# Kernel tuning notes

Measured on AMD Instinct MI355X. Metric: run time of the kernel, lower is better.

## Reference

```python
import jax, jax.numpy as jnp
import numpy as np

DIM = 768
HEADS = 12
HEAD_DIM = DIM // HEADS
SCALE = HEAD_DIM ** -0.5


def setup_inputs() -> dict:
    key = jax.random.key(0)
    k1, k2, k3, k4 = jax.random.split(key, 4)
    x = jax.random.normal(k1, (1, 4096, DIM), dtype=jnp.float32)
    # qkv: Linear(dim, 3*dim), bias=False
    W_qkv = jax.random.normal(k2, (DIM, 3 * DIM), dtype=jnp.float32) * (DIM ** -0.5)
    # proj: Linear(dim, dim) with bias
    W_proj = jax.random.normal(k3, (DIM, DIM), dtype=jnp.float32) * (DIM ** -0.5)
    b_proj = jax.random.normal(k4, (DIM,), dtype=jnp.float32) * 0.01
    return {"x": x, "W_qkv": W_qkv, "W_proj": W_proj, "b_proj": b_proj}


def reference(x, W_qkv, W_proj, b_proj):
    b, n, d = x.shape
    qkv = x @ W_qkv                                  # [b, n, 3d]
    q, k, v = jnp.split(qkv, 3, axis=-1)             # each [b, n, d]
    # split heads: [b, n, (h hd)] -> [b, h, n, hd]
    def heads(t):
        return t.reshape(b, n, HEADS, HEAD_DIM).transpose(0, 2, 1, 3)
    q, k, v = heads(q) * SCALE, heads(k), heads(v)
    sim = jnp.einsum('bhid,bhjd->bhij', q, k)        # [b, h, n, n] -- full score matrix
    attn = jax.nn.softmax(sim, axis=-1)
    out = jnp.einsum('bhij,bhjd->bhid', attn, v)     # [b, h, n, hd]
    out = out.transpose(0, 2, 1, 3).reshape(b, n, d)  # merge heads
    return out @ W_proj + b_proj
```

## Files before the change

kernel.cpp:

```cpp
#include <hip/hip_runtime.h>
#include <math.h>

#define TOKENS 4096
#define DMODEL 768
#define NHEADS 12
#define HDIM   64
#define QKV_N  2304
#define ATTN_SCALE 0.125f
#define QSCALE_LOG2E (0.125f * 1.44269504088896340736f)

typedef __attribute__((ext_vector_type(8))) short bf16x8;
typedef __attribute__((ext_vector_type(4))) float floatx4;

__device__ __forceinline__ ushort f2bf(float f) {
    union { float f; unsigned u; } cv; cv.f = f;
    unsigned u = cv.u;
    u += 0x7fffu + ((u >> 16) & 1u);
    return (ushort)(u >> 16);
}

__device__ __forceinline__ unsigned pack_bf16_rne(float a, float b) {
    union { float f; unsigned u; } ca, cb; ca.f = a; cb.f = b;
    unsigned ua = ca.u + 0x7fffu + ((ca.u >> 16) & 1u);
    unsigned ub = cb.u + 0x7fffu + ((cb.u >> 16) & 1u);
    return __builtin_amdgcn_perm(ub, ua, 0x07060302);
}

__device__ __forceinline__ void gl2lds16(const ushort* g, ushort* l) {
    __builtin_amdgcn_global_load_lds(
        (const __attribute__((address_space(1))) void*)g,
        (__attribute__((address_space(3))) void*)l, 16, 0, 0);
}

__device__ __forceinline__ bf16x8 frag(const ushort* ls, int row, int chunk) {
    return *(const bf16x8*)(ls + row * 64 + ((chunk ^ (row & 7)) * 8));
}

__global__ __launch_bounds__(256) void cvt_bf16_kernel(
    const float* __restrict__ in, ushort* __restrict__ out, int n4)
{
    const int i = blockIdx.x * 256 + threadIdx.x;
    if (i < n4) {
        const float4 v = ((const float4*)in)[i];
        ushort4 h;
        h.x = f2bf(v.x); h.y = f2bf(v.y); h.z = f2bf(v.z); h.w = f2bf(v.w);
        ((ushort4*)out)[i] = h;
    }
}

__global__ __launch_bounds__(256) void transpose_cvt_kernel(
    const float* __restrict__ in, ushort* __restrict__ out, int R, int C)
{
    __shared__ ushort tile[32][33];
    const int tx  = threadIdx.x & 31;
    const int ty8 = threadIdx.x >> 5;
    const int c0 = blockIdx.x * 32;
    const int r0 = blockIdx.y * 32;
    #pragma unroll
    for (int p = 0; p < 4; ++p) {
        const int r = ty8 + p * 8;
        tile[r][tx] = f2bf(in[(size_t)(r0 + r) * C + c0 + tx]);
    }
    __syncthreads();
    #pragma unroll
    for (int p = 0; p < 4; ++p) {
        const int c = ty8 + p * 8;
        out[(size_t)(c0 + c) * R + r0 + tx] = tile[tx][c];
    }
}

template<int NT>
__device__ __forceinline__ void gemm_body_async(
    const ushort* __restrict__ A, const ushort* __restrict__ Bt, int K,
    int m0, int n0, floatx4 acc[4][NT], ushort* ls)
{
    ushort* lsA = ls;
    ushort* lsB = ls + 8192;

    const int tid  = threadIdx.x;
    const int lane = tid & 63;
    const int wave = tid >> 6;
    const int wm = wave >> 1, wn = wave & 1;
    const int quad = lane >> 4, l16 = lane & 15;

    const int lrow = lane >> 3;
    const int csw  = ((lane & 7) ^ lrow) * 8;

    const ushort* gA = A  + (size_t)(m0 + wave * 32 + lrow) * K + csw;
    const ushort* gB = Bt + (size_t)(n0 + wave * NT * 8 + lrow) * K + csw;
    ushort* lA = lsA + (wave * 32) * 64;
    ushort* lB = lsB + (wave * NT * 8) * 64;

    for (int k0 = 0; k0 < K; k0 += 64) {
        __syncthreads();
        #pragma unroll
        for (int p = 0; p < 4; ++p)
            gl2lds16(gA + (size_t)p * 8 * K + k0, lA + p * 8 * 64);
        #pragma unroll
        for (int p = 0; p < NT; ++p)
            gl2lds16(gB + (size_t)p * 8 * K + k0, lB + p * 8 * 64);
        __syncthreads();

        #pragma unroll
        for (int ks = 0; ks < 2; ++ks) {
            bf16x8 af[4], bfr[NT];
            #pragma unroll
            for (int mt = 0; mt < 4; ++mt)
                af[mt] = frag(lsA, wm * 64 + mt * 16 + l16, ks * 4 + quad);
            #pragma unroll
            for (int nt = 0; nt < NT; ++nt)
                bfr[nt] = frag(lsB, wn * NT * 16 + nt * 16 + l16, ks * 4 + quad);
            #pragma unroll
            for (int mt = 0; mt < 4; ++mt)
                #pragma unroll
                for (int nt = 0; nt < NT; ++nt)
                    acc[mt][nt] = __builtin_amdgcn_mfma_f32_16x16x32_bf16(
                        af[mt], bfr[nt], acc[mt][nt], 0, 0, 0);
        }
    }
}

__global__ __launch_bounds__(256) void gemm_qkv_mfma(
    const ushort* __restrict__ Xb, const ushort* __restrict__ Wt,
    ushort* __restrict__ Qb, ushort* __restrict__ Kb, ushort* __restrict__ Vt)
{
    __shared__ __align__(16) ushort ls[16384];
    const int m0 = blockIdx.y * 128;
    const int n0 = blockIdx.x * 128;

    floatx4 acc[4][4] = {};
    gemm_body_async<4>(Xb, Wt, DMODEL, m0, n0, acc, ls);

    const int tid  = threadIdx.x;
    const int lane = tid & 63;
    const int wave = tid >> 6;
    const int wm = wave >> 1, wn = wave & 1;
    const int quad = lane >> 4, l16 = lane & 15;

    if (n0 < 2 * DMODEL) {
        const float scale = (n0 < DMODEL) ? QSCALE_LOG2E : 1.0f;
        ushort* outp = (n0 < DMODEL) ? Qb : Kb;
        const int colg = (n0 < DMODEL) ? n0 : n0 - DMODEL;
        #pragma unroll
        for (int p = 0; p < 2; ++p) {
            __syncthreads();
            if (wm == p) {
                #pragma unroll
                for (int mt = 0; mt < 4; ++mt)
                    #pragma unroll
                    for (int nt = 0; nt < 4; ++nt) {
                        const int row = mt * 16 + quad * 4;
                        const int col = wn * 64 + nt * 16 + l16;
                        #pragma unroll
                        for (int r = 0; r < 4; ++r)
                            ls[(row + r) * 136 + col] = f2bf(acc[mt][nt][r] * scale);
                    }
            }
            __syncthreads();
            #pragma unroll
            for (int p2 = 0; p2 < 4; ++p2) {
                const int row = (tid >> 4) + p2 * 16;
                const int c8  = (tid & 15) * 8;
                *(uint4*)(outp + (size_t)(m0 + p * 64 + row) * DMODEL + colg + c8) =
                    *(const uint4*)(ls + row * 136 + c8);
            }
        }
    } else {
        const int hd0 = n0 - 2 * DMODEL;
        #pragma unroll
        for (int p = 0; p < 2; ++p) {
            __syncthreads();
            if (wn == p) {
                #pragma unroll
                for (int mt = 0; mt < 4; ++mt)
                    #pragma unroll
                    for (int nt = 0; nt < 4; ++nt) {
                        const int hd  = nt * 16 + l16;
                        const int tok = wm * 64 + mt * 16 + quad * 4;
                        #pragma unroll
                        for (int r = 0; r < 4; ++r)
                            ls[hd * 136 + tok + r] = f2bf(acc[mt][nt][r]);
                    }
            }
            __syncthreads();
            #pragma unroll
            for (int p2 = 0; p2 < 4; ++p2) {
                const int row = (tid >> 4) + p2 * 16;
                const int c8  = (tid & 15) * 8;
                *(uint4*)(Vt + (size_t)(hd0 + p * 64 + row) * TOKENS + m0 + c8) =
                    *(const uint4*)(ls + row * 136 + c8);
            }
        }
    }
}

__global__ __launch_bounds__(256) void gemm_proj_mfma(
    const ushort* __restrict__ Ab, const ushort* __restrict__ Wt,
    const float* __restrict__ bias, float* __restrict__ out)
{
    __shared__ __align__(16) ushort ls[12288];
    const int m0 = blockIdx.y * 128;
    const int n0 = blockIdx.x * 64;

    floatx4 acc[4][2] = {};
    gemm_body_async<2>(Ab, Wt, DMODEL, m0, n0, acc, ls);

    const int lane = threadIdx.x & 63;
    const int wave = threadIdx.x >> 6;
    const int wm = wave >> 1, wn = wave & 1;
    const int quad = lane >> 4, l16 = lane & 15;
    const int row0 = m0 + wm * 64 + quad * 4;
    const int col0 = n0 + wn * 32;

    #pragma unroll
    for (int nt = 0; nt < 2; ++nt) {
        const int col = col0 + nt * 16 + l16;
        const float bv = bias[col];
        #pragma unroll
        for (int mt = 0; mt < 4; ++mt)
            #pragma unroll
            for (int r = 0; r < 4; ++r)
                out[(size_t)(row0 + mt * 16 + r) * DMODEL + col] =
                    acc[mt][nt][r] + bv;
    }
}

__global__ __launch_bounds__(256) void attn_mfma_kernel(
    const ushort* __restrict__ Qb, const ushort* __restrict__ Kb,
    const ushort* __restrict__ Vt, ushort* __restrict__ attn_out)
{
    __shared__ __align__(16) ushort lds[20480];

    const int tid  = threadIdx.x;
    const int wave = tid >> 6;
    const int lane = tid & 63;
    const int quad = lane >> 4;
    const int l16  = lane & 15;
    const int sw   = (l16 & 7);
    const int h    = blockIdx.y;
    const int i0   = blockIdx.x * 64;

    const ushort* qbase = Qb + (size_t)(i0 + wave * 16 + l16) * DMODEL + h * HDIM;
    const bf16x8 qf0 = *(const bf16x8*)(qbase + quad * 8);
    const bf16x8 qf1 = *(const bf16x8*)(qbase + 32 + quad * 8);

    bf16x8 ones;
    #pragma unroll
    for (int i = 0; i < 8; ++i) ones[i] = (short)0x3F80;

    floatx4 O[4] = {{0.f,0.f,0.f,0.f},{0.f,0.f,0.f,0.f},{0.f,0.f,0.f,0.f},{0.f,0.f,0.f,0.f}};
    floatx4 Ol = {0.f, 0.f, 0.f, 0.f};

    ushort* pw = lds + 16384 + wave * 1024 + l16 * 64;

    const int lrow = lane >> 3;
    const int csw  = ((lane & 7) ^ lrow) * 8;
    const ushort* gK = Kb + (size_t)(wave * 16 + lrow) * DMODEL + h * HDIM + csw;
    const ushort* gV = Vt + (size_t)(h * HDIM + wave * 16 + lrow) * TOKENS + csw;

    #pragma unroll
    for (int p = 0; p < 2; ++p) {
        gl2lds16(gK + (size_t)p * 8 * DMODEL, lds + (wave * 16 + p * 8) * 64);
        gl2lds16(gV + (size_t)p * 8 * TOKENS, lds + 8192 + (wave * 16 + p * 8) * 64);
    }

    for (int j0 = 0; j0 < TOKENS; j0 += 64) {
        const int cur = (j0 >> 6) & 1;
        ushort* Ks = lds + cur * 4096;
        ushort* Vs = lds + 8192 + cur * 4096;
        ushort* Kn = lds + (1 - cur) * 4096;
        ushort* Vn = lds + 8192 + (1 - cur) * 4096;

        __syncthreads();

        if (j0 + 64 < TOKENS) {
            #pragma unroll
            for (int p = 0; p < 2; ++p) {
                gl2lds16(gK + (size_t)(j0 + 64) * DMODEL + (size_t)p * 8 * DMODEL,
                         Kn + (wave * 16 + p * 8) * 64);
                gl2lds16(gV + (size_t)(j0 + 64) + (size_t)p * 8 * TOKENS,
                         Vn + (wave * 16 + p * 8) * 64);
            }
        }

        floatx4 Sv[4];
        #pragma unroll
        for (int jt = 0; jt < 4; ++jt) {
            const bf16x8 k0 = frag(Ks, jt * 16 + l16, quad);
            const bf16x8 k1 = frag(Ks, jt * 16 + l16, 4 + quad);
            floatx4 s = {0.f, 0.f, 0.f, 0.f};
            s = __builtin_amdgcn_mfma_f32_16x16x32_bf16(k0, qf0, s, 0, 0, 0);
            s = __builtin_amdgcn_mfma_f32_16x16x32_bf16(k1, qf1, s, 0, 0, 0);
            Sv[jt] = s;
        }

        #pragma unroll
        for (int jt = 0; jt < 4; ++jt) {
            const float p0 = __builtin_amdgcn_exp2f(Sv[jt][0]);
            const float p1 = __builtin_amdgcn_exp2f(Sv[jt][1]);
            const float p2 = __builtin_amdgcn_exp2f(Sv[jt][2]);
            const float p3 = __builtin_amdgcn_exp2f(Sv[jt][3]);
            uint2 val;
            val.x = pack_bf16_rne(p0, p1);
            val.y = pack_bf16_rne(p2, p3);
            const int chunk = jt * 2 + (quad >> 1);
            *(uint2*)(pw + ((chunk ^ sw) * 8) + (quad & 1) * 4) = val;
        }

        const bf16x8 pf0 = *(const bf16x8*)(pw + ((quad ^ sw) * 8));
        const bf16x8 pf1 = *(const bf16x8*)(pw + (((4 + quad) ^ sw) * 8));

        Ol = __builtin_amdgcn_mfma_f32_16x16x32_bf16(pf0, ones, Ol, 0, 0, 0);
        Ol = __builtin_amdgcn_mfma_f32_16x16x32_bf16(pf1, ones, Ol, 0, 0, 0);

        #pragma unroll
        for (int nt = 0; nt < 4; ++nt) {
            const bf16x8 v0 = frag(Vs, nt * 16 + l16, quad);
            const bf16x8 v1 = frag(Vs, nt * 16 + l16, 4 + quad);
            O[nt] = __builtin_amdgcn_mfma_f32_16x16x32_bf16(pf0, v0, O[nt], 0, 0, 0);
            O[nt] = __builtin_amdgcn_mfma_f32_16x16x32_bf16(pf1, v1, O[nt], 0, 0, 0);
        }
    }

    float linv[4];
    #pragma unroll
    for (int r = 0; r < 4; ++r) linv[r] = __builtin_amdgcn_rcpf(Ol[r]);

    const int orow0 = i0 + wave * 16 + quad * 4;
    #pragma unroll
    for (int nt = 0; nt < 4; ++nt) {
        const int d = h * HDIM + nt * 16 + l16;
        #pragma unroll
        for (int r = 0; r < 4; ++r)
            attn_out[(size_t)(orow0 + r) * DMODEL + d] = f2bf(O[nt][r] * linv[r]);
    }
}

extern "C" void kernel_launch(void* const* d_in, const int* in_sizes, int n_in,
                              void* d_out, int out_size, void* d_ws, size_t ws_size,
                              hipStream_t stream)
{
    const float* x     = (const float*)d_in[0];
    const float* Wqkv  = (const float*)d_in[1];
    const float* Wproj = (const float*)d_in[2];
    const float* bproj = (const float*)d_in[3];
    float* out = (float*)d_out;

    ushort* Xb     = (ushort*)d_ws;
    ushort* WqkvT  = Xb    + (size_t)TOKENS * DMODEL;
    ushort* WprojT = WqkvT + (size_t)QKV_N * DMODEL;
    ushort* Qb     = WprojT + (size_t)DMODEL * DMODEL;
    ushort* Kb     = Qb    + (size_t)TOKENS * DMODEL;
    ushort* Vt     = Kb    + (size_t)TOKENS * DMODEL;
    ushort* attn   = Vt    + (size_t)TOKENS * DMODEL;

    cvt_bf16_kernel<<<dim3(TOKENS * DMODEL / 4 / 256), 256, 0, stream>>>(
        x, Xb, TOKENS * DMODEL / 4);
    transpose_cvt_kernel<<<dim3(QKV_N / 32, DMODEL / 32), 256, 0, stream>>>(
        Wqkv, WqkvT, DMODEL, QKV_N);
    transpose_cvt_kernel<<<dim3(DMODEL / 32, DMODEL / 32), 256, 0, stream>>>(
        Wproj, WprojT, DMODEL, DMODEL);

    gemm_qkv_mfma<<<dim3(QKV_N / 128, TOKENS / 128), 256, 0, stream>>>(
        Xb, WqkvT, Qb, Kb, Vt);

    attn_mfma_kernel<<<dim3(TOKENS / 64, NHEADS), 256, 0, stream>>>(
        Qb, Kb, Vt, attn);

    gemm_proj_mfma<<<dim3(DMODEL / 64, TOKENS / 128), 256, 0, stream>>>(
        attn, WprojT, bproj, out);
}
```

Before: 214.9 us.

## Restructure attention so one wave processes all 64 query rows per block

The attention kernel now launches single-wave blocks. Each wave handles all four 16-row query tiles, so every K and V fragment read from LDS is reused across four query tiles instead of one. Block-level __syncthreads is replaced by explicit s_waitcnt vmcnt waits on the asynchronous global-to-LDS copies, since only one wave touches the shared buffers. The cost is fewer resident waves (768 in total), more registers per wave and less latency hiding, which may leave SIMDs underused.

```diff
diff --git a/kernel.cpp b/kernel.cpp
--- a/kernel.cpp
+++ b/kernel.cpp
@@ -225,114 +225,140 @@
     }
 }
 
-__global__ __launch_bounds__(256) void attn_mfma_kernel(
+__global__ __launch_bounds__(64) void attn_mfma_kernel(
     const ushort* __restrict__ Qb, const ushort* __restrict__ Kb,
     const ushort* __restrict__ Vt, ushort* __restrict__ attn_out)
 {
     __shared__ __align__(16) ushort lds[20480];
 
-    const int tid  = threadIdx.x;
-    const int wave = tid >> 6;
-    const int lane = tid & 63;
+    const int lane = threadIdx.x;
     const int quad = lane >> 4;
     const int l16  = lane & 15;
-    const int sw   = (l16 & 7);
     const int h    = blockIdx.y;
     const int i0   = blockIdx.x * 64;
 
-    const ushort* qbase = Qb + (size_t)(i0 + wave * 16 + l16) * DMODEL + h * HDIM;
-    const bf16x8 qf0 = *(const bf16x8*)(qbase + quad * 8);
-    const bf16x8 qf1 = *(const bf16x8*)(qbase + 32 + quad * 8);
+    bf16x8 qf[4][2];
+    #pragma unroll
+    for (int qt = 0; qt < 4; ++qt)
+        #pragma unroll
+        for (int ks = 0; ks < 2; ++ks)
+            qf[qt][ks] = *(const bf16x8*)(Qb +
+                (size_t)(i0 + qt * 16 + l16) * DMODEL + h * HDIM + ks * 32 + quad * 8);
 
     bf16x8 ones;
     #pragma unroll
     for (int i = 0; i < 8; ++i) ones[i] = (short)0x3F80;
 
-    floatx4 O[4] = {{0.f,0.f,0.f,0.f},{0.f,0.f,0.f,0.f},{0.f,0.f,0.f,0.f},{0.f,0.f,0.f,0.f}};
-    floatx4 Ol = {0.f, 0.f, 0.f, 0.f};
-
-    ushort* pw = lds + 16384 + wave * 1024 + l16 * 64;
+    floatx4 O[4][4];
+    #pragma unroll
+    for (int mt = 0; mt < 4; ++mt)
+        #pragma unroll
+        for (int nt = 0; nt < 4; ++nt) O[mt][nt] = (floatx4){0.f, 0.f, 0.f, 0.f};
+    floatx4 Ol[4];
+    #pragma unroll
+    for (int mt = 0; mt < 4; ++mt) Ol[mt] = (floatx4){0.f, 0.f, 0.f, 0.f};
+
+    ushort* Pb = lds + 16384;
 
     const int lrow = lane >> 3;
     const int csw  = ((lane & 7) ^ lrow) * 8;
-    const ushort* gK = Kb + (size_t)(wave * 16 + lrow) * DMODEL + h * HDIM + csw;
-    const ushort* gV = Vt + (size_t)(h * HDIM + wave * 16 + lrow) * TOKENS + csw;
-
-    #pragma unroll
-    for (int p = 0; p < 2; ++p) {
-        gl2lds16(gK + (size_t)p * 8 * DMODEL, lds + (wave * 16 + p * 8) * 64);
-        gl2lds16(gV + (size_t)p * 8 * TOKENS, lds + 8192 + (wave * 16 + p * 8) * 64);
+    const ushort* gK = Kb + (size_t)lrow * DMODEL + h * HDIM + csw;
+    const ushort* gV = Vt + (size_t)(h * HDIM + lrow) * TOKENS + csw;
+
+    #pragma unroll
+    for (int p = 0; p < 8; ++p) {
+        gl2lds16(gK + (size_t)p * 8 * DMODEL, lds + p * 8 * 64);
+        gl2lds16(gV + (size_t)p * 8 * TOKENS, lds + 8192 + p * 8 * 64);
     }
 
     for (int j0 = 0; j0 < TOKENS; j0 += 64) {
         const int cur = (j0 >> 6) & 1;
-        ushort* Ks = lds + cur * 4096;
-        ushort* Vs = lds + 8192 + cur * 4096;
-        ushort* Kn = lds + (1 - cur) * 4096;
-        ushort* Vn = lds + 8192 + (1 - cur) * 4096;
-
-        __syncthreads();
+        const ushort* Ks = lds + cur * 4096;
+        const ushort* Vs = lds + 8192 + cur * 4096;
 
         if (j0 + 64 < TOKENS) {
-            #pragma unroll
-            for (int p = 0; p < 2; ++p) {
+            ushort* Kn = lds + (1 - cur) * 4096;
+            ushort* Vn = lds + 8192 + (1 - cur) * 4096;
+            #pragma unroll
+            for (int p = 0; p < 8; ++p) {
                 gl2lds16(gK + (size_t)(j0 + 64) * DMODEL + (size_t)p * 8 * DMODEL,
-                         Kn + (wave * 16 + p * 8) * 64);
+                         Kn + p * 8 * 64);
                 gl2lds16(gV + (size_t)(j0 + 64) + (size_t)p * 8 * TOKENS,
-                         Vn + (wave * 16 + p * 8) * 64);
-            }
-        }
-
-        floatx4 Sv[4];
+                         Vn + p * 8 * 64);
+            }
+            asm volatile("s_waitcnt vmcnt(16)" ::: "memory");
+        } else {
+            asm volatile("s_waitcnt vmcnt(0)" ::: "memory");
+        }
+
+        floatx4 Sv[4][4];
         #pragma unroll
         for (int jt = 0; jt < 4; ++jt) {
             const bf16x8 k0 = frag(Ks, jt * 16 + l16, quad);
             const bf16x8 k1 = frag(Ks, jt * 16 + l16, 4 + quad);
-            floatx4 s = {0.f, 0.f, 0.f, 0.f};
-            s = __builtin_amdgcn_mfma_f32_16x16x32_bf16(k0, qf0, s, 0, 0, 0);
-            s = __builtin_amdgcn_mfma_f32_16x16x32_bf16(k1, qf1, s, 0, 0, 0);
-            Sv[jt] = s;
-        }
-
-        #pragma unroll
-        for (int jt = 0; jt < 4; ++jt) {
-            const float p0 = __builtin_amdgcn_exp2f(Sv[jt][0]);
-            const float p1 = __builtin_amdgcn_exp2f(Sv[jt][1]);
-            const float p2 = __builtin_amdgcn_exp2f(Sv[jt][2]);
-            const float p3 = __builtin_amdgcn_exp2f(Sv[jt][3]);
-            uint2 val;
-            val.x = pack_bf16_rne(p0, p1);
-            val.y = pack_bf16_rne(p2, p3);
-            const int chunk = jt * 2 + (quad >> 1);
-            *(uint2*)(pw + ((chunk ^ sw) * 8) + (quad & 1) * 4) = val;
-        }
-
-        const bf16x8 pf0 = *(const bf16x8*)(pw + ((quad ^ sw) * 8));
-        const bf16x8 pf1 = *(const bf16x8*)(pw + (((4 + quad) ^ sw) * 8));
-
-        Ol = __builtin_amdgcn_mfma_f32_16x16x32_bf16(pf0, ones, Ol, 0, 0, 0);
-        Ol = __builtin_amdgcn_mfma_f32_16x16x32_bf16(pf1, ones, Ol, 0, 0, 0);
+            #pragma unroll
+            for (int qt = 0; qt < 4; ++qt) {
+                floatx4 s = {0.f, 0.f, 0.f, 0.f};
+                s = __builtin_amdgcn_mfma_f32_16x16x32_bf16(k0, qf[qt][0], s, 0, 0, 0);
+                s = __builtin_amdgcn_mfma_f32_16x16x32_bf16(k1, qf[qt][1], s, 0, 0, 0);
+                Sv[jt][qt] = s;
+            }
+        }
+
+        #pragma unroll
+        for (int jt = 0; jt < 4; ++jt)
+            #pragma unroll
+            for (int qt = 0; qt < 4; ++qt) {
+                const float p0 = __builtin_amdgcn_exp2f(Sv[jt][qt][0]);
+                const float p1 = __builtin_amdgcn_exp2f(Sv[jt][qt][1]);
+                const float p2 = __builtin_amdgcn_exp2f(Sv[jt][qt][2]);
+                const float p3 = __builtin_amdgcn_exp2f(Sv[jt][qt][3]);
+                uint2 val;
+                val.x = pack_bf16_rne(p0, p1);
+                val.y = pack_bf16_rne(p2, p3);
+                const int q = qt * 16 + l16;
+                const int c = jt * 2 + (quad >> 1);
+                *(uint2*)(Pb + (q * 8 + (c ^ (q & 7))) * 8 + (quad & 1) * 4) = val;
+            }
+
+        bf16x8 pf[4][2];
+        #pragma unroll
+        for (int mt = 0; mt < 4; ++mt) {
+            pf[mt][0] = frag(Pb, mt * 16 + l16, quad);
+            pf[mt][1] = frag(Pb, mt * 16 + l16, 4 + quad);
+        }
+
+        #pragma unroll
+        for (int mt = 0; mt < 4; ++mt) {
+            Ol[mt] = __builtin_amdgcn_mfma_f32_16x16x32_bf16(pf[mt][0], ones, Ol[mt], 0, 0, 0);
+            Ol[mt] = __builtin_amdgcn_mfma_f32_16x16x32_bf16(pf[mt][1], ones, Ol[mt], 0, 0, 0);
+        }
 
         #pragma unroll
         for (int nt = 0; nt < 4; ++nt) {
             const bf16x8 v0 = frag(Vs, nt * 16 + l16, quad);
             const bf16x8 v1 = frag(Vs, nt * 16 + l16, 4 + quad);
-            O[nt] = __builtin_amdgcn_mfma_f32_16x16x32_bf16(pf0, v0, O[nt], 0, 0, 0);
-            O[nt] = __builtin_amdgcn_mfma_f32_16x16x32_bf16(pf1, v1, O[nt], 0, 0, 0);
-        }
-    }
-
-    float linv[4];
-    #pragma unroll
-    for (int r = 0; r < 4; ++r) linv[r] = __builtin_amdgcn_rcpf(Ol[r]);
-
-    const int orow0 = i0 + wave * 16 + quad * 4;
-    #pragma unroll
-    for (int nt = 0; nt < 4; ++nt) {
-        const int d = h * HDIM + nt * 16 + l16;
-        #pragma unroll
-        for (int r = 0; r < 4; ++r)
-            attn_out[(size_t)(orow0 + r) * DMODEL + d] = f2bf(O[nt][r] * linv[r]);
+            #pragma unroll
+            for (int mt = 0; mt < 4; ++mt) {
+                O[mt][nt] = __builtin_amdgcn_mfma_f32_16x16x32_bf16(pf[mt][0], v0, O[mt][nt], 0, 0, 0);
+                O[mt][nt] = __builtin_amdgcn_mfma_f32_16x16x32_bf16(pf[mt][1], v1, O[mt][nt], 0, 0, 0);
+            }
+        }
+    }
+
+    #pragma unroll
+    for (int mt = 0; mt < 4; ++mt) {
+        float linv[4];
+        #pragma unroll
+        for (int r = 0; r < 4; ++r) linv[r] = __builtin_amdgcn_rcpf(Ol[mt][r]);
+        const int row0 = i0 + mt * 16 + quad * 4;
+        #pragma unroll
+        for (int nt = 0; nt < 4; ++nt) {
+            const int d = h * HDIM + nt * 16 + l16;
+            #pragma unroll
+            for (int r = 0; r < 4; ++r)
+                attn_out[(size_t)(row0 + r) * DMODEL + d] = f2bf(O[mt][nt][r] * linv[r]);
+        }
     }
 }
 
@@ -364,7 +390,7 @@
     gemm_qkv_mfma<<<dim3(QKV_N / 128, TOKENS / 128), 256, 0, stream>>>(
         Xb, WqkvT, Qb, Kb, Vt);
 
-    attn_mfma_kernel<<<dim3(TOKENS / 64, NHEADS), 256, 0, stream>>>(
+    attn_mfma_kernel<<<dim3(TOKENS / 64, NHEADS), 64, 0, stream>>>(
         Qb, Kb, Vt, attn);
 
     gemm_proj_mfma<<<dim3(DMODEL / 64, TOKENS / 128), 256, 0, stream>>>(
```

Measured after the change: 240.4 us. 11.9% more time.

## Keep P in registers using 16x16x16 MFMA and permuted V layout in LDS

Applied to the files above, without the earlier changes.

The attention kernel no longer round-trips the softmax probabilities through LDS. The exp'd scores stay in registers as bf16x4 fragments and feed 16x16x16 bf16 MFMAs directly. To match that operand layout, V tiles are loaded through registers and scattered into a permuted, padded LDS layout (row stride 68) instead of using direct global-to-LDS copies. This removes the P write/read and one LDS buffer, but it doubles the MFMA count at half the K depth and adds register-staged V stores plus a sync placed at the end of each iteration.

```diff
diff --git a/kernel.cpp b/kernel.cpp
--- a/kernel.cpp
+++ b/kernel.cpp
@@ -10,6 +10,7 @@
 #define QSCALE_LOG2E (0.125f * 1.44269504088896340736f)
 
 typedef __attribute__((ext_vector_type(8))) short bf16x8;
+typedef __attribute__((ext_vector_type(4))) short bf16x4;
 typedef __attribute__((ext_vector_type(4))) float floatx4;
 
 __device__ __forceinline__ ushort f2bf(float f) {
@@ -229,14 +230,13 @@
     const ushort* __restrict__ Qb, const ushort* __restrict__ Kb,
     const ushort* __restrict__ Vt, ushort* __restrict__ attn_out)
 {
-    __shared__ __align__(16) ushort lds[20480];
+    __shared__ __align__(16) ushort lds[16896];
 
     const int tid  = threadIdx.x;
     const int wave = tid >> 6;
     const int lane = tid & 63;
     const int quad = lane >> 4;
     const int l16  = lane & 15;
-    const int sw   = (l16 & 7);
     const int h    = blockIdx.y;
     const int i0   = blockIdx.x * 64;
 
@@ -244,43 +244,55 @@
     const bf16x8 qf0 = *(const bf16x8*)(qbase + quad * 8);
     const bf16x8 qf1 = *(const bf16x8*)(qbase + 32 + quad * 8);
 
-    bf16x8 ones;
-    #pragma unroll
-    for (int i = 0; i < 8; ++i) ones[i] = (short)0x3F80;
+    bf16x4 ones4;
+    #pragma unroll
+    for (int i = 0; i < 4; ++i) ones4[i] = (short)0x3F80;
 
     floatx4 O[4] = {{0.f,0.f,0.f,0.f},{0.f,0.f,0.f,0.f},{0.f,0.f,0.f,0.f},{0.f,0.f,0.f,0.f}};
     floatx4 Ol = {0.f, 0.f, 0.f, 0.f};
-
-    ushort* pw = lds + 16384 + wave * 1024 + l16 * 64;
 
     const int lrow = lane >> 3;
     const int csw  = ((lane & 7) ^ lrow) * 8;
     const ushort* gK = Kb + (size_t)(wave * 16 + lrow) * DMODEL + h * HDIM + csw;
-    const ushort* gV = Vt + (size_t)(h * HDIM + wave * 16 + lrow) * TOKENS + csw;
-
-    #pragma unroll
-    for (int p = 0; p < 2; ++p) {
+
+    const int vrow = wave * 16 + (lane >> 2);
+    const ushort* gV = Vt + (size_t)(h * HDIM + vrow) * TOKENS + (lane & 3) * 8;
+    const int kg0 = 2 * (lane & 3);
+    const int wr  = vrow * 68;
+    const int woff0 = 16 * (kg0 & 3) + 4 * (kg0 >> 2);
+    const int woff1 = 16 * ((kg0 + 1) & 3) + 4 * ((kg0 + 1) >> 2);
+    const int woff2 = 16 * (kg0 & 3) + 4 * ((kg0 + 8) >> 2);
+    const int woff3 = 16 * ((kg0 + 1) & 3) + 4 * ((kg0 + 9) >> 2);
+
+    #pragma unroll
+    for (int p = 0; p < 2; ++p)
         gl2lds16(gK + (size_t)p * 8 * DMODEL, lds + (wave * 16 + p * 8) * 64);
-        gl2lds16(gV + (size_t)p * 8 * TOKENS, lds + 8192 + (wave * 16 + p * 8) * 64);
-    }
+    {
+        const uint4 v1 = *(const uint4*)(gV);
+        const uint4 v2 = *(const uint4*)(gV + 32);
+        ushort* Vp = lds + 8192;
+        *(uint2*)(Vp + wr + woff0) = make_uint2(v1.x, v1.y);
+        *(uint2*)(Vp + wr + woff1) = make_uint2(v1.z, v1.w);
+        *(uint2*)(Vp + wr + woff2) = make_uint2(v2.x, v2.y);
+        *(uint2*)(Vp + wr + woff3) = make_uint2(v2.z, v2.w);
+    }
+    __syncthreads();
 
     for (int j0 = 0; j0 < TOKENS; j0 += 64) {
         const int cur = (j0 >> 6) & 1;
-        ushort* Ks = lds + cur * 4096;
-        ushort* Vs = lds + 8192 + cur * 4096;
-        ushort* Kn = lds + (1 - cur) * 4096;
-        ushort* Vn = lds + 8192 + (1 - cur) * 4096;
-
-        __syncthreads();
-
-        if (j0 + 64 < TOKENS) {
-            #pragma unroll
-            for (int p = 0; p < 2; ++p) {
+        const ushort* Ks = lds + cur * 4096;
+        const ushort* Vp = lds + 8192 + cur * 4352;
+        const bool more = (j0 + 64 < TOKENS);
+
+        uint4 v1, v2;
+        if (more) {
+            ushort* Kn = lds + (1 - cur) * 4096;
+            #pragma unroll
+            for (int p = 0; p < 2; ++p)
                 gl2lds16(gK + (size_t)(j0 + 64) * DMODEL + (size_t)p * 8 * DMODEL,
                          Kn + (wave * 16 + p * 8) * 64);
-                gl2lds16(gV + (size_t)(j0 + 64) + (size_t)p * 8 * TOKENS,
-                         Vn + (wave * 16 + p * 8) * 64);
-            }
+            v1 = *(const uint4*)(gV + (j0 + 64));
+            v2 = *(const uint4*)(gV + (j0 + 64) + 32);
         }
 
         floatx4 Sv[4];
@@ -294,32 +306,41 @@
             Sv[jt] = s;
         }
 
+        bf16x4 pf[4];
         #pragma unroll
         for (int jt = 0; jt < 4; ++jt) {
             const float p0 = __builtin_amdgcn_exp2f(Sv[jt][0]);
             const float p1 = __builtin_amdgcn_exp2f(Sv[jt][1]);
             const float p2 = __builtin_amdgcn_exp2f(Sv[jt][2]);
             const float p3 = __builtin_amdgcn_exp2f(Sv[jt][3]);
-            uint2 val;
-            val.x = pack_bf16_rne(p0, p1);
-            val.y = pack_bf16_rne(p2, p3);
-            const int chunk = jt * 2 + (quad >> 1);
-            *(uint2*)(pw + ((chunk ^ sw) * 8) + (quad & 1) * 4) = val;
-        }
-
-        const bf16x8 pf0 = *(const bf16x8*)(pw + ((quad ^ sw) * 8));
-        const bf16x8 pf1 = *(const bf16x8*)(pw + (((4 + quad) ^ sw) * 8));
-
-        Ol = __builtin_amdgcn_mfma_f32_16x16x32_bf16(pf0, ones, Ol, 0, 0, 0);
-        Ol = __builtin_amdgcn_mfma_f32_16x16x32_bf16(pf1, ones, Ol, 0, 0, 0);
+            union { uint2 u; bf16x4 h; } cv;
+            cv.u.x = pack_bf16_rne(p0, p1);
+            cv.u.y = pack_bf16_rne(p2, p3);
+            pf[jt] = cv.h;
+        }
+
+        #pragma unroll
+        for (int jt = 0; jt < 4; ++jt)
+            Ol = __builtin_amdgcn_mfma_f32_16x16x16bf16_1k(pf[jt], ones4, Ol, 0, 0, 0);
 
         #pragma unroll
         for (int nt = 0; nt < 4; ++nt) {
-            const bf16x8 v0 = frag(Vs, nt * 16 + l16, quad);
-            const bf16x8 v1 = frag(Vs, nt * 16 + l16, 4 + quad);
-            O[nt] = __builtin_amdgcn_mfma_f32_16x16x32_bf16(pf0, v0, O[nt], 0, 0, 0);
-            O[nt] = __builtin_amdgcn_mfma_f32_16x16x32_bf16(pf1, v1, O[nt], 0, 0, 0);
-        }
+            const int rbase = (nt * 16 + l16) * 68 + 16 * quad;
+            #pragma unroll
+            for (int jt = 0; jt < 4; ++jt) {
+                const bf16x4 v = *(const bf16x4*)(Vp + rbase + 4 * jt);
+                O[nt] = __builtin_amdgcn_mfma_f32_16x16x16bf16_1k(pf[jt], v, O[nt], 0, 0, 0);
+            }
+        }
+
+        if (more) {
+            ushort* Vn = lds + 8192 + (1 - cur) * 4352;
+            *(uint2*)(Vn + wr + woff0) = make_uint2(v1.x, v1.y);
+            *(uint2*)(Vn + wr + woff1) = make_uint2(v1.z, v1.w);
+            *(uint2*)(Vn + wr + woff2) = make_uint2(v2.x, v2.y);
+            *(uint2*)(Vn + wr + woff3) = make_uint2(v2.z, v2.w);
+        }
+        __syncthreads();
     }
 
     float linv[4];
```

Result: slower. 223.1 us (+3.8%).
